# Optimization experiments

Measured on AMD Instinct MI355X. Metric: run time of the kernel, lower is better.

The kernel has to match this reference:

```python
import jax, jax.numpy as jnp
import numpy as np

N_NODES = 50000
N_EDGES = 800000
D_IN = 512
D_HID = 256


def gcn_conv(x, W, b, src, dst, n_nodes):
    """PyG-style GCNConv: self-loops + symmetric normalization.
    x: [N, d_in], W: [d_in, d_out], b: [d_out], src/dst: [E] (already include self-loops? no -> add here)
    """
    loops = jnp.arange(n_nodes, dtype=src.dtype)
    src_f = jnp.concatenate([src, loops])  # [E+N]
    dst_f = jnp.concatenate([dst, loops])
    deg = jax.ops.segment_sum(jnp.ones_like(dst_f, dtype=x.dtype), dst_f,
                              num_segments=n_nodes)  # [N]
    dinv = jnp.where(deg > 0, jax.lax.rsqrt(deg), 0.0)
    norm = dinv[src_f] * dinv[dst_f]  # [E+N]
    h = x @ W  # [N, d_out] -- dense GEMM
    msg = h[src_f] * norm[:, None]  # gather + scale, [E+N, d_out]
    out = jax.ops.segment_sum(msg, dst_f, num_segments=n_nodes)  # scatter-add
    return out + b


def setup_inputs() -> dict:
    key = jax.random.key(0)
    k1, k2, k3, k4, k5 = jax.random.split(key, 5)
    x = jax.random.normal(k1, (N_NODES, D_IN), dtype=jnp.float32)
    edge_index = jax.random.randint(k2, (2, N_EDGES), 0, N_NODES, dtype=jnp.int32)
    # Glorot-ish init for weights
    W1 = jax.random.normal(k3, (D_IN, D_HID), dtype=jnp.float32) / np.sqrt(D_IN)
    W2 = jax.random.normal(k4, (D_HID, D_HID), dtype=jnp.float32) / np.sqrt(D_HID)
    b1 = jnp.zeros((D_HID,), dtype=jnp.float32)
    b2 = jnp.zeros((D_HID,), dtype=jnp.float32)
    return {"x": x, "edge_index": edge_index, "W1": W1, "b1": b1, "W2": W2, "b2": b2}


def reference(x, edge_index, W1, b1, W2, b2):
    n_nodes = x.shape[0]
    src, dst = edge_index[0], edge_index[1]
    h = jax.nn.relu(gcn_conv(x, W1, b1, src, dst, n_nodes))
    h = gcn_conv(h, W2, b2, src, dst, n_nodes)
    # edge-level gather-dot scoring
    score = jnp.einsum('ed,ed->e', h[src], h[dst])  # [E]
    prob_edge = jax.nn.sigmoid(score)
    return prob_edge
```

## Files before the change

kernel.cpp:

```cpp
#include <hip/hip_runtime.h>
#include <stdint.h>

#define D_IN 512
#define D_HID 256

typedef __attribute__((ext_vector_type(8))) short bf16x8;
typedef __attribute__((ext_vector_type(8))) unsigned short u16x8;
typedef __attribute__((ext_vector_type(4))) float f32x4;

__device__ __forceinline__ float b2f(unsigned short u) {
    union { float f; uint32_t i; } x; x.i = ((uint32_t)u) << 16; return x.f;
}
__device__ __forceinline__ unsigned short f2b(float f) {
    union { float f; uint32_t i; } x; x.f = f;
    uint32_t i = x.i;
    uint32_t r = (i + 0x7FFFu + ((i >> 16) & 1u)) >> 16;
    return (unsigned short)r;
}

__device__ __forceinline__ void async_copy16(const unsigned short* g, unsigned short* lds) {
    __builtin_amdgcn_global_load_lds((const __attribute__((address_space(1))) unsigned int*)g,
                                     (__attribute__((address_space(3))) unsigned int*)lds,
                                     16, 0, 0);
}

__global__ __launch_bounds__(256) void detect_dtype_kernel(const ushort4* __restrict__ raw,
                                                           int n4, int* __restrict__ flag) {
    int i = blockIdx.x * blockDim.x + threadIdx.x;
    int hit = 0;
    if (i < n4) {
        ushort4 u = raw[i];
        hit = ((((u.x >> 7) & 0xFF) == 0xFF) || (((u.y >> 7) & 0xFF) == 0xFF) ||
               (((u.z >> 7) & 0xFF) == 0xFF) || (((u.w >> 7) & 0xFF) == 0xFF)) ? 1 : 0;
    }
    unsigned long long b = __ballot(hit);
    if ((threadIdx.x & 63) == 0 && b != 0ULL) atomicOr(flag, 1);
}

__global__ void hist_kernel(const int* __restrict__ dst, int* __restrict__ counts, int E) {
    int e = blockIdx.x * blockDim.x + threadIdx.x;
    if (e < E) atomicAdd(&counts[dst[e]], 1);
}

__global__ __launch_bounds__(256) void partial_sum_kernel(const int* __restrict__ counts,
        int* __restrict__ partial, int n) {
    __shared__ int sh[4];
    int b = blockIdx.x;
    int lane = threadIdx.x & 63, wv = threadIdx.x >> 6;
    int s = 0;
    for (int j = threadIdx.x; j < 1024; j += 256) {
        int i = b * 1024 + j;
        s += (i < n) ? counts[i] : 0;
    }
#pragma unroll
    for (int off = 32; off > 0; off >>= 1) s += __shfl_down(s, off, 64);
    if (lane == 0) sh[wv] = s;
    __syncthreads();
    if (threadIdx.x == 0) partial[b] = sh[0] + sh[1] + sh[2] + sh[3];
}

__global__ void scan_partials_kernel(int* __restrict__ partial, int nb,
                                     int* __restrict__ indptr, int N) {
    int lane = threadIdx.x & 63;
    int orig = (lane < nb) ? partial[lane] : 0;
    int v = orig;
#pragma unroll
    for (int off = 1; off < 64; off <<= 1) {
        int u = __shfl(v, lane - off, 64);
        if (lane >= off) v += u;
    }
    int tot = __shfl(v, nb - 1, 64);
    if (lane < nb) partial[lane] = v - orig;
    if (lane == 0) indptr[N] = tot;
}

__global__ __launch_bounds__(1024) void scan_chunk_kernel(const int* __restrict__ counts,
        const int* __restrict__ partial, int* __restrict__ indptr, int* __restrict__ cursor,
        float* __restrict__ dinv, int n) {
    __shared__ int sh[1024];
    int b = blockIdx.x;
    int i = b * 1024 + threadIdx.x;
    int v = (i < n) ? counts[i] : 0;
    sh[threadIdx.x] = v;
    __syncthreads();
    for (int off = 1; off < 1024; off <<= 1) {
        int t = (threadIdx.x >= off) ? sh[threadIdx.x - off] : 0;
        __syncthreads();
        sh[threadIdx.x] += t;
        __syncthreads();
    }
    if (i < n) {
        int e = partial[b] + sh[threadIdx.x] - v;
        indptr[i] = e;
        cursor[i] = e;
        dinv[i] = rsqrtf((float)(v + 1));
    }
}

__global__ void scatter_kernel(const int* __restrict__ dst,
                               int* __restrict__ cursor, int* __restrict__ eid_at,
                               int* __restrict__ pos_of, int E) {
    int e = blockIdx.x * blockDim.x + threadIdx.x;
    if (e < E) {
        int d = dst[e];
        int pos = atomicAdd(&cursor[d], 1);
        eid_at[pos] = e;
        pos_of[e] = pos;
    }
}

__global__ __launch_bounds__(256) void csr_fill_kernel(const int* __restrict__ eid_at,
        const int* __restrict__ src, const int* __restrict__ dst,
        int* __restrict__ csr_src, int* __restrict__ csr_dst, int E) {
    int p = blockIdx.x * blockDim.x + threadIdx.x;
    if (p < E) {
        int e = eid_at[p];
        csr_src[p] = src[e];
        csr_dst[p] = dst[e];
    }
}

__global__ __launch_bounds__(256) void wpack_kernel(const void* __restrict__ W,
        unsigned short* __restrict__ Wp, int K, const int* __restrict__ flag) {
    int t = blockIdx.x * blockDim.x + threadIdx.x;
    int total = (K >> 6) * 2 * 16 * 64;
    if (t >= total) return;
    int lane = t & 63;
    int c = (t >> 6) & 15;
    int h = (t >> 10) & 1;
    int kk = t >> 11;
    int n = c * 16 + (lane & 15);
    int k0 = kk * 64 + h * 32 + (lane >> 4) * 8;
    bool f32 = (*flag != 0);
    u16x8 o;
#pragma unroll
    for (int j = 0; j < 8; ++j) {
        float v = f32 ? ((const float*)W)[(size_t)(k0 + j) * 256 + n]
                      : b2f(((const unsigned short*)W)[(size_t)(k0 + j) * 256 + n]);
        o[j] = f2b(v);
    }
    *(u16x8*)(Wp + (size_t)t * 8) = o;
}

template<int K, bool MF32>
__global__ __launch_bounds__(256) void gemm_bf16(const void* __restrict__ Ain,
        const unsigned short* __restrict__ Wp, unsigned short* __restrict__ C, int M,
        const int* __restrict__ flag) {
    __shared__ unsigned short As[2][64 * 64];
    constexpr int NK = K / 64;
    int t = threadIdx.x;
    int lane = t & 63, wv = t >> 6;
    int n0 = lane & 15, grp = lane >> 4;
    int row0 = blockIdx.x * 64;

    int srow = wv * 16 + (lane >> 3);
    int segp = lane & 7;

    f32x4 acc[4][4];
#pragma unroll
    for (int rt = 0; rt < 4; ++rt)
#pragma unroll
        for (int ct = 0; ct < 4; ++ct) acc[rt][ct] = (f32x4){0.f, 0.f, 0.f, 0.f};

    auto compute_tile = [&](int kk, const unsigned short* Abuf) {
        bf16x8 bw[4][2];
#pragma unroll
        for (int ct = 0; ct < 4; ++ct)
#pragma unroll
            for (int h = 0; h < 2; ++h)
                bw[ct][h] = *(const bf16x8*)(Wp +
                    ((size_t)(((kk * 2 + h) * 16) + (wv * 4 + ct)) * 64 + lane) * 8);
#pragma unroll
        for (int rt = 0; rt < 4; ++rt) {
            int r = rt * 16 + n0;
#pragma unroll
            for (int h = 0; h < 2; ++h) {
                int sp = (h * 4 + grp + r) & 7;
                bf16x8 a = *(const bf16x8*)(Abuf + r * 64 + sp * 8);
#pragma unroll
                for (int ct = 0; ct < 4; ++ct)
                    acc[rt][ct] = __builtin_amdgcn_mfma_f32_16x16x32_bf16(a, bw[ct][h],
                                                                          acc[rt][ct], 0, 0, 0);
            }
        }
    };

    bool f32src = MF32 && (*flag != 0);
    if (f32src) {
        const float* A = (const float*)Ain;
        auto stage_f32 = [&](int buf, const float4* pr) {
#pragma unroll
            for (int j = 0; j < 2; ++j) {
                u16x8 o;
#pragma unroll
                for (int q = 0; q < 4; ++q) {
                    o[q]     = f2b(pr[j * 2 + 0][q]);
                    o[q + 4] = f2b(pr[j * 2 + 1][q]);
                }
                *(u16x8*)(&As[buf][0] + wv * 1024 + j * 512 + lane * 8) = o;
            }
        };
        auto load_f32 = [&](int kof, float4* pr) {
#pragma unroll
            for (int j = 0; j < 2; ++j) {
                int row = srow + j * 8;
                int s = (segp - row) & 7;
                const float* g = A + (size_t)min(row0 + row, M - 1) * K + kof + s * 8;
                pr[j * 2 + 0] = *(const float4*)(g);
                pr[j * 2 + 1] = *(const float4*)(g + 4);
            }
        };
        float4 pr[4];
        load_f32(0, pr);
        stage_f32(0, pr);
        for (int kk = 0; kk < NK; ++kk) {
            int cur = kk & 1;
            if (kk + 1 < NK) load_f32((kk + 1) * 64, pr);
            asm volatile("s_waitcnt lgkmcnt(0)" ::: "memory");
            __builtin_amdgcn_s_barrier();
            compute_tile(kk, &As[cur][0]);
            if (kk + 1 < NK) stage_f32(cur ^ 1, pr);
        }
    } else {
        const unsigned short* A = (const unsigned short*)Ain;
#pragma unroll
        for (int j = 0; j < 2; ++j) {
            int row = srow + j * 8;
            int s = (segp - row) & 7;
            const unsigned short* g = A + (size_t)min(row0 + row, M - 1) * K + s * 8;
            async_copy16(g, &As[0][0] + wv * 1024 + j * 512);
        }
        asm volatile("s_waitcnt vmcnt(0)" ::: "memory");
        __builtin_amdgcn_s_barrier();
        for (int kk = 0; kk < NK; ++kk) {
            int cur = kk & 1;
            if (kk + 1 < NK) {
                int kof = (kk + 1) * 64;
#pragma unroll
                for (int j = 0; j < 2; ++j) {
                    int row = srow + j * 8;
                    int s = (segp - row) & 7;
                    const unsigned short* g = A + (size_t)min(row0 + row, M - 1) * K + kof + s * 8;
                    async_copy16(g, &As[cur ^ 1][0] + wv * 1024 + j * 512);
                }
            }
            compute_tile(kk, &As[cur][0]);
            asm volatile("s_waitcnt vmcnt(0)" ::: "memory");
            __builtin_amdgcn_s_barrier();
        }
    }
#pragma unroll
    for (int rt = 0; rt < 4; ++rt) {
#pragma unroll
        for (int ct = 0; ct < 4; ++ct) {
#pragma unroll
            for (int reg = 0; reg < 4; ++reg) {
                int row = row0 + rt * 16 + grp * 4 + reg;
                if (row < M)
                    C[(size_t)row * 256 + (wv * 4 + ct) * 16 + n0] = f2b(acc[rt][ct][reg]);
            }
        }
    }
}

__global__ __launch_bounds__(256) void aggregate_kernel(const unsigned short* __restrict__ h,
        const int* __restrict__ indptr, const int* __restrict__ csr_src,
        const float* __restrict__ dinv, const void* __restrict__ bias,
        unsigned short* __restrict__ out, int n, int do_relu, const int* __restrict__ flag) {
    int wave = threadIdx.x >> 6;
    int lane = threadIdx.x & 63;
    int half = lane >> 5;
    int hl = lane & 31;
    int v = blockIdx.x * 4 + wave;
    if (v >= n) return;
    int beg = indptr[v];
    int end = indptr[v + 1];
    float dv = dinv[v];

    float acc[8];
    if (half == 0) {
        u16x8 hv = *(const u16x8*)(h + (size_t)v * 256 + hl * 8);
#pragma unroll
        for (int i = 0; i < 8; ++i) acc[i] = dv * b2f(hv[i]);
    } else {
#pragma unroll
        for (int i = 0; i < 8; ++i) acc[i] = 0.f;
    }

    float wA = 0.f, wB = 0.f, wC = 0.f;
    u16x8 rA = (u16x8)0, rB = (u16x8)0, rC = (u16x8)0;
    auto ld = [&](int idx, float& w, u16x8& r) {
        if (idx < end) {
            int s = csr_src[idx];
            w = dinv[s];
            r = *(const u16x8*)(h + (size_t)s * 256 + hl * 8);
        } else {
            w = 0.f;
        }
    };
    int e = beg + half;
    ld(e, wA, rA);
    ld(e + 2, wB, rB);
    ld(e + 4, wC, rC);
    while (e + 4 < end) {
#pragma unroll
        for (int i = 0; i < 8; ++i) acc[i] += wA * b2f(rA[i]);
        ld(e + 6, wA, rA);
#pragma unroll
        for (int i = 0; i < 8; ++i) acc[i] += wB * b2f(rB[i]);
        ld(e + 8, wB, rB);
#pragma unroll
        for (int i = 0; i < 8; ++i) acc[i] += wC * b2f(rC[i]);
        ld(e + 10, wC, rC);
        e += 6;
    }
#pragma unroll
    for (int i = 0; i < 8; ++i)
        acc[i] += wA * b2f(rA[i]) + wB * b2f(rB[i]) + wC * b2f(rC[i]);

#pragma unroll
    for (int i = 0; i < 8; ++i) acc[i] += __shfl_xor(acc[i], 32, 64);

    if (half == 0) {
        float bb[8];
        if (*flag != 0) {
            const float* bp = (const float*)bias + hl * 8;
#pragma unroll
            for (int i = 0; i < 8; ++i) bb[i] = bp[i];
        } else {
            const unsigned short* bp = (const unsigned short*)bias + hl * 8;
#pragma unroll
            for (int i = 0; i < 8; ++i) bb[i] = b2f(bp[i]);
        }
        u16x8 ov;
#pragma unroll
        for (int i = 0; i < 8; ++i) {
            float o = dv * acc[i] + bb[i];
            if (do_relu) o = fmaxf(o, 0.f);
            ov[i] = f2b(o);
        }
        *(u16x8*)(out + (size_t)v * 256 + hl * 8) = ov;
    }
}

__global__ __launch_bounds__(256) void edge_score_mfma(const unsigned short* __restrict__ h,
        const int* __restrict__ csr_src, const int* __restrict__ csr_dst,
        float* __restrict__ tmp, int E) {
    int lane = threadIdx.x & 63;
    int wv = threadIdx.x >> 6;
    int base = (blockIdx.x * 4 + wv) * 16;
    if (base >= E) return;
    int m = lane & 15, grp = lane >> 4;
    int e = base + m;
    int ec = min(e, E - 1);
    int s = csr_src[ec], d = csr_dst[ec];
    const unsigned short* hs = h + (size_t)s * 256 + grp * 8;
    const unsigned short* hd = h + (size_t)d * 256 + grp * 8;
    f32x4 acc = {0.f, 0.f, 0.f, 0.f};
#pragma unroll
    for (int kk = 0; kk < 8; ++kk) {
        bf16x8 a = *(const bf16x8*)(hs + kk * 32);
        bf16x8 b = *(const bf16x8*)(hd + kk * 32);
        acc = __builtin_amdgcn_mfma_f32_16x16x32_bf16(a, b, acc, 0, 0, 0);
    }
    int reg = m - grp * 4;
    if (reg >= 0 && reg < 4 && e < E) {
        float p = (reg == 0) ? acc[0] : (reg == 1) ? acc[1] : (reg == 2) ? acc[2] : acc[3];
        tmp[e] = 1.f / (1.f + __expf(-p));
    }
}

__global__ __launch_bounds__(256) void permute_out_kernel(const float* __restrict__ tmp,
        const int* __restrict__ pos_of, void* __restrict__ out, int E,
        const int* __restrict__ flag) {
    int e = blockIdx.x * blockDim.x + threadIdx.x;
    if (e >= E) return;
    float p = tmp[pos_of[e]];
    if (*flag != 0)
        ((float*)out)[e] = p;
    else
        ((unsigned short*)out)[e] = f2b(p);
}

extern "C" void kernel_launch(void* const* d_in, const int* in_sizes, int n_in,
                              void* d_out, int out_size, void* d_ws, size_t ws_size,
                              hipStream_t stream) {
    const void* x  = d_in[0];
    const int* edge_index = (const int*)d_in[1];
    const void* W1 = d_in[2];
    const void* b1 = d_in[3];
    const void* W2 = d_in[4];
    const void* b2 = d_in[5];

    const int N = in_sizes[0] / D_IN;
    const int E = in_sizes[1] / 2;
    const int* src = edge_index;
    const int* dst = edge_index + E;

    char* ws = (char*)d_ws;
    size_t off = 0;
    auto alloc = [&](size_t bytes) {
        char* p = ws + off;
        off = (off + bytes + 255) & ~(size_t)255;
        return p;
    };
    int* flag     = (int*)alloc(256);
    float* dinv   = (float*)alloc((size_t)N * 4);
    int* counts   = (int*)alloc((size_t)N * 4);
    int* indptr   = (int*)alloc((size_t)(N + 1) * 4);
    int* cursor   = (int*)alloc((size_t)N * 4);
    int* partial  = (int*)alloc(64 * 4);
    int* csr_src  = (int*)alloc((size_t)E * 4);
    int* csr_dst  = (int*)alloc((size_t)E * 4);
    int* eid_at   = (int*)alloc((size_t)E * 4);
    int* pos_of   = (int*)alloc((size_t)E * 4);
    float* ptmp   = (float*)alloc((size_t)E * 4);
    unsigned short* Wp1 = (unsigned short*)alloc((size_t)D_IN * 256 * 2);
    unsigned short* Wp2 = (unsigned short*)alloc((size_t)D_HID * 256 * 2);
    unsigned short* hA  = (unsigned short*)alloc((size_t)N * 256 * 2);
    unsigned short* hB  = (unsigned short*)alloc((size_t)N * 256 * 2);

    const int nb = (N + 1023) / 1024;

    hipMemsetAsync(flag, 0, 4, stream);
    hipMemsetAsync(counts, 0, (size_t)N * 4, stream);
    detect_dtype_kernel<<<64, 256, 0, stream>>>((const ushort4*)x, 16384, flag);
    hist_kernel<<<(E + 255) / 256, 256, 0, stream>>>(dst, counts, E);
    partial_sum_kernel<<<nb, 256, 0, stream>>>(counts, partial, N);
    scan_partials_kernel<<<1, 64, 0, stream>>>(partial, nb, indptr, N);
    scan_chunk_kernel<<<nb, 1024, 0, stream>>>(counts, partial, indptr, cursor, dinv, N);
    scatter_kernel<<<(E + 255) / 256, 256, 0, stream>>>(dst, cursor, eid_at, pos_of, E);
    csr_fill_kernel<<<(E + 255) / 256, 256, 0, stream>>>(eid_at, src, dst, csr_src, csr_dst, E);
    wpack_kernel<<<(D_IN * 32 + 255) / 256, 256, 0, stream>>>(W1, Wp1, D_IN, flag);
    wpack_kernel<<<(D_HID * 32 + 255) / 256, 256, 0, stream>>>(W2, Wp2, D_HID, flag);

    int ggrid = (N + 63) / 64;
    gemm_bf16<D_IN, true><<<ggrid, 256, 0, stream>>>(x, Wp1, hA, N, flag);
    aggregate_kernel<<<(N + 3) / 4, 256, 0, stream>>>(hA, indptr, csr_src, dinv, b1, hB, N, 1, flag);
    gemm_bf16<D_HID, false><<<ggrid, 256, 0, stream>>>(hB, Wp2, hA, N, flag);
    aggregate_kernel<<<(N + 3) / 4, 256, 0, stream>>>(hA, indptr, csr_src, dinv, b2, hB, N, 0, flag);
    edge_score_mfma<<<(E + 63) / 64, 256, 0, stream>>>(hB, csr_src, csr_dst, ptmp, E);
    permute_out_kernel<<<(E + 255) / 256, 256, 0, stream>>>(ptmp, pos_of, d_out, E, flag);
}
```

Baseline: 506.9 us.

## Fuse histogram with weight packing and merge CSR scatter into first GEMM launch

```diff
diff --git a/kernel.cpp b/kernel.cpp
--- a/kernel.cpp
+++ b/kernel.cpp
@@ -37,9 +37,44 @@
     if ((threadIdx.x & 63) == 0 && b != 0ULL) atomicOr(flag, 1);
 }
 
-__global__ void hist_kernel(const int* __restrict__ dst, int* __restrict__ counts, int E) {
-    int e = blockIdx.x * blockDim.x + threadIdx.x;
-    if (e < E) atomicAdd(&counts[dst[e]], 1);
+__device__ __forceinline__ void wpack_body(const void* __restrict__ W,
+        unsigned short* __restrict__ Wp, int K, bool f32, int t) {
+    int total = (K >> 6) * 2 * 16 * 64;
+    if (t >= total) return;
+    int lane = t & 63;
+    int c = (t >> 6) & 15;
+    int h = (t >> 10) & 1;
+    int kk = t >> 11;
+    int n = c * 16 + (lane & 15);
+    int k0 = kk * 64 + h * 32 + (lane >> 4) * 8;
+    u16x8 o;
+#pragma unroll
+    for (int j = 0; j < 8; ++j) {
+        float v = f32 ? ((const float*)W)[(size_t)(k0 + j) * 256 + n]
+                      : b2f(((const unsigned short*)W)[(size_t)(k0 + j) * 256 + n]);
+        o[j] = f2b(v);
+    }
+    *(u16x8*)(Wp + (size_t)t * 8) = o;
+}
+
+__global__ __launch_bounds__(256) void pre_fused_kernel(const int* __restrict__ dst,
+        int* __restrict__ counts, int E,
+        const void* __restrict__ W1, unsigned short* __restrict__ Wp1,
+        const void* __restrict__ W2, unsigned short* __restrict__ Wp2,
+        const int* __restrict__ flag, int histBlocks, int wp1Blocks) {
+    int b = blockIdx.x;
+    if (b < histBlocks) {
+        int e = b * 256 + threadIdx.x;
+        if (e < E) atomicAdd(&counts[dst[e]], 1);
+        return;
+    }
+    b -= histBlocks;
+    bool f32 = (*flag != 0);
+    if (b < wp1Blocks) {
+        wpack_body(W1, Wp1, D_IN, f32, b * 256 + threadIdx.x);
+    } else {
+        wpack_body(W2, Wp2, D_HID, f32, (b - wp1Blocks) * 256 + threadIdx.x);
+    }
 }
 
 __global__ __launch_bounds__(256) void partial_sum_kernel(const int* __restrict__ counts,
@@ -97,61 +132,33 @@
     }
 }
 
-__global__ void scatter_kernel(const int* __restrict__ dst,
-                               int* __restrict__ cursor, int* __restrict__ eid_at,
-                               int* __restrict__ pos_of, int E) {
-    int e = blockIdx.x * blockDim.x + threadIdx.x;
-    if (e < E) {
-        int d = dst[e];
-        int pos = atomicAdd(&cursor[d], 1);
-        eid_at[pos] = e;
-        pos_of[e] = pos;
-    }
-}
-
-__global__ __launch_bounds__(256) void csr_fill_kernel(const int* __restrict__ eid_at,
-        const int* __restrict__ src, const int* __restrict__ dst,
-        int* __restrict__ csr_src, int* __restrict__ csr_dst, int E) {
-    int p = blockIdx.x * blockDim.x + threadIdx.x;
-    if (p < E) {
-        int e = eid_at[p];
-        csr_src[p] = src[e];
-        csr_dst[p] = dst[e];
-    }
-}
-
-__global__ __launch_bounds__(256) void wpack_kernel(const void* __restrict__ W,
-        unsigned short* __restrict__ Wp, int K, const int* __restrict__ flag) {
-    int t = blockIdx.x * blockDim.x + threadIdx.x;
-    int total = (K >> 6) * 2 * 16 * 64;
-    if (t >= total) return;
-    int lane = t & 63;
-    int c = (t >> 6) & 15;
-    int h = (t >> 10) & 1;
-    int kk = t >> 11;
-    int n = c * 16 + (lane & 15);
-    int k0 = kk * 64 + h * 32 + (lane >> 4) * 8;
-    bool f32 = (*flag != 0);
-    u16x8 o;
-#pragma unroll
-    for (int j = 0; j < 8; ++j) {
-        float v = f32 ? ((const float*)W)[(size_t)(k0 + j) * 256 + n]
-                      : b2f(((const unsigned short*)W)[(size_t)(k0 + j) * 256 + n]);
-        o[j] = f2b(v);
-    }
-    *(u16x8*)(Wp + (size_t)t * 8) = o;
-}
-
-template<int K, bool MF32>
+template<int K, bool MF32, bool FUSE>
 __global__ __launch_bounds__(256) void gemm_bf16(const void* __restrict__ Ain,
         const unsigned short* __restrict__ Wp, unsigned short* __restrict__ C, int M,
-        const int* __restrict__ flag) {
+        const int* __restrict__ flag,
+        const int* __restrict__ eidx, int* __restrict__ cursor, int* __restrict__ csr_src,
+        int* __restrict__ csr_dst, int* __restrict__ pos_of, int E, int sblocks) {
     __shared__ unsigned short As[2][64 * 64];
     constexpr int NK = K / 64;
+    int bid = blockIdx.x;
+    if (FUSE) {
+        if (bid < sblocks) {
+            int e = bid * 256 + (int)threadIdx.x;
+            if (e < E) {
+                int d = eidx[(size_t)E + e];
+                int pos = atomicAdd(&cursor[d], 1);
+                csr_src[pos] = eidx[e];
+                csr_dst[pos] = d;
+                pos_of[e] = pos;
+            }
+            return;
+        }
+        bid -= sblocks;
+    }
     int t = threadIdx.x;
     int lane = t & 63, wv = t >> 6;
     int n0 = lane & 15, grp = lane >> 4;
-    int row0 = blockIdx.x * 64;
+    int row0 = bid * 64;
 
     int srow = wv * 16 + (lane >> 3);
     int segp = lane & 7;
@@ -394,7 +401,6 @@
 
     const int N = in_sizes[0] / D_IN;
     const int E = in_sizes[1] / 2;
-    const int* src = edge_index;
     const int* dst = edge_index + E;
 
     char* ws = (char*)d_ws;
@@ -412,7 +418,6 @@
     int* partial  = (int*)alloc(64 * 4);
     int* csr_src  = (int*)alloc((size_t)E * 4);
     int* csr_dst  = (int*)alloc((size_t)E * 4);
-    int* eid_at   = (int*)alloc((size_t)E * 4);
     int* pos_of   = (int*)alloc((size_t)E * 4);
     float* ptmp   = (float*)alloc((size_t)E * 4);
     unsigned short* Wp1 = (unsigned short*)alloc((size_t)D_IN * 256 * 2);
@@ -421,23 +426,25 @@
     unsigned short* hB  = (unsigned short*)alloc((size_t)N * 256 * 2);
 
     const int nb = (N + 1023) / 1024;
+    const int sblocks = (E + 255) / 256;
+    const int wp1Blocks = (D_IN * 32) / 256;
+    const int wp2Blocks = (D_HID * 32) / 256;
+    const int ggrid = (N + 63) / 64;
 
     hipMemsetAsync(flag, 0, 4, stream);
     hipMemsetAsync(counts, 0, (size_t)N * 4, stream);
     detect_dtype_kernel<<<64, 256, 0, stream>>>((const ushort4*)x, 16384, flag);
-    hist_kernel<<<(E + 255) / 256, 256, 0, stream>>>(dst, counts, E);
+    pre_fused_kernel<<<sblocks + wp1Blocks + wp2Blocks, 256, 0, stream>>>(
+        dst, counts, E, W1, Wp1, W2, Wp2, flag, sblocks, wp1Blocks);
     partial_sum_kernel<<<nb, 256, 0, stream>>>(counts, partial, N);
     scan_partials_kernel<<<1, 64, 0, stream>>>(partial, nb, indptr, N);
     scan_chunk_kernel<<<nb, 1024, 0, stream>>>(counts, partial, indptr, cursor, dinv, N);
-    scatter_kernel<<<(E + 255) / 256, 256, 0, stream>>>(dst, cursor, eid_at, pos_of, E);
-    csr_fill_kernel<<<(E + 255) / 256, 256, 0, stream>>>(eid_at, src, dst, csr_src, csr_dst, E);
-    wpack_kernel<<<(D_IN * 32 + 255) / 256, 256, 0, stream>>>(W1, Wp1, D_IN, flag);
-    wpack_kernel<<<(D_HID * 32 + 255) / 256, 256, 0, stream>>>(W2, Wp2, D_HID, flag);
-
-    int ggrid = (N + 63) / 64;
-    gemm_bf16<D_IN, true><<<ggrid, 256, 0, stream>>>(x, Wp1, hA, N, flag);
+
+    gemm_bf16<D_IN, true, true><<<sblocks + ggrid, 256, 0, stream>>>(
+        x, Wp1, hA, N, flag, edge_index, cursor, csr_src, csr_dst, pos_of, E, sblocks);
     aggregate_kernel<<<(N + 3) / 4, 256, 0, stream>>>(hA, indptr, csr_src, dinv, b1, hB, N, 1, flag);
-    gemm_bf16<D_HID, false><<<ggrid, 256, 0, stream>>>(hB, Wp2, hA, N, flag);
+    gemm_bf16<D_HID, false, false><<<ggrid, 256, 0, stream>>>(
+        hB, Wp2, hA, N, flag, nullptr, nullptr, nullptr, nullptr, nullptr, 0, 0);
     aggregate_kernel<<<(N + 3) / 4, 256, 0, stream>>>(hA, indptr, csr_src, dinv, b2, hB, N, 0, flag);
     edge_score_mfma<<<(E + 63) / 64, 256, 0, stream>>>(hB, csr_src, csr_dst, ptmp, E);
     permute_out_kernel<<<(E + 255) / 256, 256, 0, stream>>>(ptmp, pos_of, d_out, E, flag);
```

Result: faster. 476.7 us (-6.0%).
